# Kernel tuning notes

Hardware: AMD Instinct MI355X
Metric: run time of the kernel (lower is better)

The kernel has to match this reference:

```python
import jax, jax.numpy as jnp
import numpy as np

N, E, D, S, H, R = 16384, 262144, 64, 16, 8, 64
DH = D * H  # 512, tp2 output width (num_heads * node feature dim)
DOUT = 64
EPS = 1e-6


def _layernorm(x, g, b):
    mu = jnp.mean(x, axis=-1, keepdims=True)
    var = jnp.mean(jnp.square(x - mu), axis=-1, keepdims=True)
    return (x - mu) * jax.lax.rsqrt(var + EPS) * g + b


def setup_inputs() -> dict:
    key = jax.random.key(0)
    ks = jax.random.split(key, 16)
    rn = lambda k, shape, scale: jax.random.normal(k, shape, dtype=jnp.float32) * scale
    inp = {
        "node_fea": rn(ks[0], (N, D), 1.0),
        "edge_sh": rn(ks[1], (E, S), 1.0),
        "edge_length_embedding": rn(ks[2], (E, R), 1.0),
        "edge_src": jax.random.randint(ks[3], (E,), 0, N, dtype=jnp.int32),
        "edge_dst": jax.random.randint(ks[4], (E,), 0, N, dtype=jnp.int32),
        "batch": jnp.zeros((N,), dtype=jnp.int32),
        # pre_lin: Linear(D + D + R -> D)
        "W_pre": rn(ks[5], (D + D + R, D), 1.0 / np.sqrt(D + D + R)),
        "b_pre": jnp.zeros((D,), jnp.float32),
        # tp2 (EquiConv): tensor-product weights + radial gating MLP 64->64->DH
        "W_tp2": rn(ks[6], (D, S, DH), 1.0 / np.sqrt(D * S)),
        "r1": rn(ks[7], (R, R), 1.0 / np.sqrt(R)),
        "rb1": jnp.zeros((R,), jnp.float32),
        "r2": rn(ks[8], (R, DH), 1.0 / np.sqrt(R)),
        "rb2": jnp.zeros((DH,), jnp.float32),
        # lin_alpha: 64 -> 64 LN SiLU -> 64 LN SiLU -> H
        "a1": rn(ks[9], (R, R), 1.0 / np.sqrt(R)),
        "ab1": jnp.zeros((R,), jnp.float32),
        "g1": jnp.ones((R,), jnp.float32),
        "be1": jnp.zeros((R,), jnp.float32),
        "a2": rn(ks[10], (R, R), 1.0 / np.sqrt(R)),
        "ab2": jnp.zeros((R,), jnp.float32),
        "g2": jnp.ones((R,), jnp.float32),
        "be2": jnp.zeros((R,), jnp.float32),
        "a3": rn(ks[11], (R, H), 1.0 / np.sqrt(R)),
        "ab3": jnp.zeros((H,), jnp.float32),
        # lin: Linear(D*H -> DOUT)
        "W_lin": rn(ks[12], (DH, DOUT), 1.0 / np.sqrt(DH)),
        "b_lin": jnp.zeros((DOUT,), jnp.float32),
    }
    return inp


def reference(node_fea, edge_sh, edge_length_embedding, edge_src, edge_dst, batch,
              W_pre, b_pre, W_tp2, r1, rb1, r2, rb2,
              a1, ab1, g1, be1, a2, ab2, g2, be2, a3, ab3, W_lin, b_lin):
    n_nodes = node_fea.shape[0]
    # gather src/dst node features, concat radial embedding, pre_lin
    msg = jnp.concatenate(
        [node_fea[edge_src], node_fea[edge_dst], edge_length_embedding], axis=-1)
    msg = msg @ W_pre + b_pre  # [E, D]
    # EquiConv tp2: (msg tensor-product sh) contracted with learned weights,
    # gated per output channel by a radial MLP.
    gate = jax.nn.silu(edge_length_embedding @ r1 + rb1) @ r2 + rb2  # [E, DH]
    xs = jnp.einsum('ei,es->eis', msg, edge_sh).reshape(msg.shape[0], D * S)
    value = (xs @ W_tp2.reshape(D * S, DH)) * gate  # [E, DH]
    value = value.reshape(value.shape[0], H, D)  # [E, H, D]
    # attention logits from radial embedding
    h = jax.nn.silu(_layernorm(edge_length_embedding @ a1 + ab1, g1, be1))
    h = jax.nn.silu(_layernorm(h @ a2 + ab2, g2, be2))
    alpha = h @ a3 + ab3  # [E, H]
    # per-destination-node softmax over incoming edges
    m = jax.ops.segment_max(alpha, edge_dst, num_segments=n_nodes)
    ea = jnp.exp(alpha - m[edge_dst])
    denom = jax.ops.segment_sum(ea, edge_dst, num_segments=n_nodes)
    alpha = ea / denom[edge_dst]  # [E, H]
    # weight values and scatter-sum into destination nodes
    edge_fea = value * alpha[..., None]  # [E, H, D]
    node_agg = jax.ops.segment_sum(edge_fea, edge_dst, num_segments=n_nodes)
    out = node_agg.reshape(n_nodes, H * D) @ W_lin + b_lin  # [N, DOUT]
    return out
```

## Files before the change

### kernel.cpp

```cpp
#include <hip/hip_runtime.h>
#include <cstdint>
#include <cstddef>


typedef unsigned int u32;
typedef unsigned short u16;
typedef __attribute__((ext_vector_type(8))) short short8;
typedef __attribute__((ext_vector_type(4))) float f32x4;
typedef __attribute__((ext_vector_type(4))) u32 u32x4;

__device__ __forceinline__ float bf2f(u16 u){ return __uint_as_float(((u32)u)<<16); }
__device__ __forceinline__ u16 f2bf(float f){
  u32 i = __float_as_uint(f);
  u32 r = i + 0x7FFFu + ((i>>16)&1u);
  return (u16)(r>>16);
}
__device__ __forceinline__ u32 pk2(float a, float b){
  return (u32)f2bf(a) | ((u32)f2bf(b)<<16);
}
__device__ __forceinline__ u32 cvtpk(float a, float b){
  u32 r;
  asm("v_cvt_pk_bf16_f32 %0, %1, %2" : "=v"(r) : "v"(a), "v"(b));
  return r;
}
__device__ __forceinline__ void atomAddF(float* p, float v){
  asm volatile("global_atomic_add_f32 %0, %1, off" :: "v"(p), "v"(v) : "memory");
}
__device__ __forceinline__ void gl2lds(const void* g, void* l){
  __builtin_amdgcn_global_load_lds((const __attribute__((address_space(1))) u32*)g,
                                   (__attribute__((address_space(3))) u32*)l, 16, 0, 0);
}
__device__ __forceinline__ float decm(u32 k){
  u32 b = (k & 0x80000000u) ? (k & 0x7FFFFFFFu) : ~k;
  return __uint_as_float(b);
}

__global__ void k_prep(float* __restrict__ out, const float* __restrict__ bl,
                       u32* __restrict__ mkey, float* __restrict__ denom,
                       const float* __restrict__ W2, u16* __restrict__ w2t,
                       const float* __restrict__ r2, u16* __restrict__ r2t,
                       const float* __restrict__ Wl, u16* __restrict__ wlt)
{
  int t = blockIdx.x*256 + threadIdx.x;
  if (t < 1048576){ out[t] = bl[t&63]; return; }
  t -= 1048576;
  if (t < 131072){ mkey[t] = 0u; return; }
  t -= 131072;
  if (t < 131072){ denom[t] = 0.f; return; }
  t -= 131072;
  if (t < 65536){
    int o = t & 511, kc = t >> 9;
    u32x4 v;
    v.x = pk2(W2[(size_t)(kc*8+0)*512+o], W2[(size_t)(kc*8+1)*512+o]);
    v.y = pk2(W2[(size_t)(kc*8+2)*512+o], W2[(size_t)(kc*8+3)*512+o]);
    v.z = pk2(W2[(size_t)(kc*8+4)*512+o], W2[(size_t)(kc*8+5)*512+o]);
    v.w = pk2(W2[(size_t)(kc*8+6)*512+o], W2[(size_t)(kc*8+7)*512+o]);
    *(u32x4*)((char*)w2t + (size_t)o*2048 + kc*16) = v;
    return;
  }
  t -= 65536;
  if (t < 4096){
    int o = t & 511, kc = t >> 9;
    u32x4 v;
    v.x = pk2(r2[(size_t)(kc*8+0)*512+o], r2[(size_t)(kc*8+1)*512+o]);
    v.y = pk2(r2[(size_t)(kc*8+2)*512+o], r2[(size_t)(kc*8+3)*512+o]);
    v.z = pk2(r2[(size_t)(kc*8+4)*512+o], r2[(size_t)(kc*8+5)*512+o]);
    v.w = pk2(r2[(size_t)(kc*8+6)*512+o], r2[(size_t)(kc*8+7)*512+o]);
    *(u32x4*)((char*)r2t + (size_t)o*128 + kc*16) = v;
    return;
  }
  t -= 4096;
  {
    int j = t & 63, kc = t >> 6;
    u32x4 v;
    v.x = pk2(Wl[(size_t)(kc*8+0)*64+j], Wl[(size_t)(kc*8+1)*64+j]);
    v.y = pk2(Wl[(size_t)(kc*8+2)*64+j], Wl[(size_t)(kc*8+3)*64+j]);
    v.z = pk2(Wl[(size_t)(kc*8+4)*64+j], Wl[(size_t)(kc*8+5)*64+j]);
    v.w = pk2(Wl[(size_t)(kc*8+6)*64+j], Wl[(size_t)(kc*8+7)*64+j]);
    *(u32x4*)((char*)wlt + (size_t)j*1024 + kc*16) = v;
  }
}

#define GEMV4(ACC, X, WBASE)                                                       \
  { const float* w_ = (WBASE);                                                     \
    _Pragma("unroll") for (int j=0;j<64;j++) ACC[j] = fmaf((X).x, w_[j],     ACC[j]); \
    _Pragma("unroll") for (int j=0;j<64;j++) ACC[j] = fmaf((X).y, w_[64+j],  ACC[j]); \
    _Pragma("unroll") for (int j=0;j<64;j++) ACC[j] = fmaf((X).z, w_[128+j], ACC[j]); \
    _Pragma("unroll") for (int j=0;j<64;j++) ACC[j] = fmaf((X).w, w_[192+j], ACC[j]); }

__global__ __launch_bounds__(256) void k_msg(
    const float* __restrict__ nf, const float* __restrict__ eleg,
    const int* __restrict__ esrc, const int* __restrict__ edst,
    const float* __restrict__ Wp, const float* __restrict__ bp,
    const float* __restrict__ r1, const float* __restrict__ rb1,
    u16* __restrict__ msgb, u16* __restrict__ hgb)
{
  const int e = blockIdx.x*256 + threadIdx.x;
  const int src = esrc[e];
  const int dst = edst[e];
  const float4* sr4 = (const float4*)(nf + (size_t)src*64);
  const float4* dr4 = (const float4*)(nf + (size_t)dst*64);
  const float4* er4 = (const float4*)(eleg + (size_t)e*64);

  float acc[64];
  #pragma unroll
  for (int j=0;j<64;j++) acc[j] = bp[j];
  for (int ic=0; ic<16; ++ic){ float4 x = sr4[ic]; GEMV4(acc, x, Wp + ic*256); }
  for (int ic=0; ic<16; ++ic){ float4 x = dr4[ic]; GEMV4(acc, x, Wp + 4096 + ic*256); }
  for (int ic=0; ic<16; ++ic){ float4 x = er4[ic]; GEMV4(acc, x, Wp + 8192 + ic*256); }
  {
    u32x4* md = (u32x4*)(msgb + (size_t)e*64);
    #pragma unroll
    for (int c=0;c<8;c++){
      u32x4 v;
      v.x = cvtpk(acc[8*c+0],acc[8*c+1]); v.y = cvtpk(acc[8*c+2],acc[8*c+3]);
      v.z = cvtpk(acc[8*c+4],acc[8*c+5]); v.w = cvtpk(acc[8*c+6],acc[8*c+7]);
      md[c] = v;
    }
  }
  #pragma unroll
  for (int j=0;j<64;j++) acc[j] = rb1[j];
  for (int ic=0; ic<16; ++ic){ float4 x = er4[ic]; GEMV4(acc, x, r1 + ic*256); }
  #pragma unroll
  for (int j=0;j<64;j++) acc[j] = acc[j] / (1.f + __expf(-acc[j]));
  {
    u32x4* hd = (u32x4*)(hgb + (size_t)e*64);
    #pragma unroll
    for (int c=0;c<8;c++){
      u32x4 v;
      v.x = cvtpk(acc[8*c+0],acc[8*c+1]); v.y = cvtpk(acc[8*c+2],acc[8*c+3]);
      v.z = cvtpk(acc[8*c+4],acc[8*c+5]); v.w = cvtpk(acc[8*c+6],acc[8*c+7]);
      hd[c] = v;
    }
  }
}

__global__ __launch_bounds__(256) void k_attn(
    const float* __restrict__ eleg, const int* __restrict__ edst,
    const float* __restrict__ a1, const float* __restrict__ ab1,
    const float* __restrict__ g1, const float* __restrict__ be1,
    const float* __restrict__ a2, const float* __restrict__ ab2,
    const float* __restrict__ g2, const float* __restrict__ be2,
    const float* __restrict__ a3, const float* __restrict__ ab3,
    float* __restrict__ eab, u32* __restrict__ mkey)
{
  const int e = blockIdx.x*256 + threadIdx.x;
  const int dst = edst[e];
  const float4* er4 = (const float4*)(eleg + (size_t)e*64);

  float u[64];
  #pragma unroll
  for (int j=0;j<64;j++) u[j] = ab1[j];
  for (int ic=0; ic<16; ++ic){ float4 x = er4[ic]; GEMV4(u, x, a1 + ic*256); }
  {
    float s = 0.f;
    #pragma unroll
    for (int j=0;j<64;j++) s += u[j];
    float mu = s * 0.015625f;
    float s2 = 0.f;
    #pragma unroll
    for (int j=0;j<64;j++){ float d = u[j]-mu; s2 = fmaf(d,d,s2); }
    float rs = rsqrtf(s2*0.015625f + 1e-6f);
    #pragma unroll
    for (int j=0;j<64;j++){
      float y = (u[j]-mu)*rs*g1[j] + be1[j];
      u[j] = y / (1.f + __expf(-y));
    }
  }
  float v[64];
  #pragma unroll
  for (int j=0;j<64;j++) v[j] = ab2[j];
  #pragma unroll
  for (int i=0;i<64;i++){
    float x = u[i];
    const float* w = a2 + i*64;
    #pragma unroll
    for (int j=0;j<64;j++) v[j] = fmaf(x, w[j], v[j]);
  }
  {
    float s = 0.f;
    #pragma unroll
    for (int j=0;j<64;j++) s += v[j];
    float mu = s * 0.015625f;
    float s2 = 0.f;
    #pragma unroll
    for (int j=0;j<64;j++){ float d = v[j]-mu; s2 = fmaf(d,d,s2); }
    float rs = rsqrtf(s2*0.015625f + 1e-6f);
    #pragma unroll
    for (int j=0;j<64;j++){
      float y = (v[j]-mu)*rs*g2[j] + be2[j];
      v[j] = y / (1.f + __expf(-y));
    }
  }
  float l[8];
  #pragma unroll
  for (int h=0;h<8;h++) l[h] = ab3[h];
  #pragma unroll
  for (int i=0;i<64;i++){
    float x = v[i];
    #pragma unroll
    for (int h=0;h<8;h++) l[h] = fmaf(x, a3[i*8+h], l[h]);
  }
  float4* ld = (float4*)(eab + (size_t)e*8);
  ld[0] = make_float4(l[0],l[1],l[2],l[3]);
  ld[1] = make_float4(l[4],l[5],l[6],l[7]);
  #pragma unroll
  for (int h=0;h<8;h++){
    u32 b = __float_as_uint(l[h]);
    u32 k = (b & 0x80000000u) ? ~b : (b | 0x80000000u);
    atomicMax(&mkey[(size_t)dst*8 + h], k);
  }
}

__global__ void k_ea(const int* __restrict__ edst, float* __restrict__ eab,
                     const u32* __restrict__ mkey, float* __restrict__ denom)
{
  int e = blockIdx.x*256 + threadIdx.x;
  int dst = edst[e];
  float4 l0 = ((const float4*)(eab + (size_t)e*8))[0];
  float4 l1 = ((const float4*)(eab + (size_t)e*8))[1];
  uint4 k0 = ((const uint4*)(mkey + (size_t)dst*8))[0];
  uint4 k1 = ((const uint4*)(mkey + (size_t)dst*8))[1];
  float e0 = __expf(l0.x - decm(k0.x));
  float e1 = __expf(l0.y - decm(k0.y));
  float e2 = __expf(l0.z - decm(k0.z));
  float e3 = __expf(l0.w - decm(k0.w));
  float e4 = __expf(l1.x - decm(k1.x));
  float e5 = __expf(l1.y - decm(k1.y));
  float e6 = __expf(l1.z - decm(k1.z));
  float e7 = __expf(l1.w - decm(k1.w));
  ((float4*)(eab + (size_t)e*8))[0] = make_float4(e0,e1,e2,e3);
  ((float4*)(eab + (size_t)e*8))[1] = make_float4(e4,e5,e6,e7);
  float* dn = denom + (size_t)dst*8;
  atomAddF(dn+0,e0); atomAddF(dn+1,e1); atomAddF(dn+2,e2); atomAddF(dn+3,e3);
  atomAddF(dn+4,e4); atomAddF(dn+5,e5); atomAddF(dn+6,e6); atomAddF(dn+7,e7);
}

__global__ void k_norm(const int* __restrict__ edst, float* __restrict__ eab,
                       const float* __restrict__ denom)
{
  int e = blockIdx.x*256 + threadIdx.x;
  int dst = edst[e];
  float4 a0 = ((const float4*)(eab + (size_t)e*8))[0];
  float4 a1 = ((const float4*)(eab + (size_t)e*8))[1];
  float4 d0 = ((const float4*)(denom + (size_t)dst*8))[0];
  float4 d1 = ((const float4*)(denom + (size_t)dst*8))[1];
  ((float4*)(eab + (size_t)e*8))[0] = make_float4(a0.x/d0.x, a0.y/d0.y, a0.z/d0.z, a0.w/d0.w);
  ((float4*)(eab + (size_t)e*8))[1] = make_float4(a1.x/d1.x, a1.y/d1.y, a1.z/d1.z, a1.w/d1.w);
}

#define FORM_A(KSP, AN) {                                                        \
  float f0_ = bf2f((u16)((mrow[KSP]>>mshift)&0xFFFFu));                          \
  u32x4 w0_, w1_;                                                                \
  w0_.x=cvtpk(f0_*shr[0], f0_*shr[1]);  w0_.y=cvtpk(f0_*shr[2], f0_*shr[3]);     \
  w0_.z=cvtpk(f0_*shr[4], f0_*shr[5]);  w0_.w=cvtpk(f0_*shr[6], f0_*shr[7]);     \
  w1_.x=cvtpk(f0_*shr[8], f0_*shr[9]);  w1_.y=cvtpk(f0_*shr[10],f0_*shr[11]);    \
  w1_.z=cvtpk(f0_*shr[12],f0_*shr[13]); w1_.w=cvtpk(f0_*shr[14],f0_*shr[15]);    \
  char* b_ = (AN) + erow*128; int r7_ = erow&7;                                  \
  *(u32x4*)(b_ + (((t4*2+0)^r7_)*16)) = w0_;                                     \
  *(u32x4*)(b_ + (((t4*2+1)^r7_)*16)) = w1_; }

#define STAGE_B(KSP, BN) {                                                       \
  _Pragma("unroll")                                                              \
  for (int c_=0;c_<2;c_++){                                                      \
    int cid_=c_*512+tid, row_=cid_>>3, ch_=cid_&7;                               \
    gl2lds((const char*)w2t + (size_t)(j0+row_)*2048 + (KSP)*128 + ((ch_^(row_&7))*16), \
           (BN) + c_*8192 + wub);                                                \
  } }

__global__ __launch_bounds__(512,2) void k_fused(
    const u16* __restrict__ msgb, const float* __restrict__ shg,
    const u16* __restrict__ w2t, const u16* __restrict__ hgb,
    const u16* __restrict__ r2t, const float* __restrict__ rb2,
    const float* __restrict__ alpha, const u16* __restrict__ wlt,
    const int* __restrict__ edst, float* __restrict__ out)
{
  __shared__ char lds[65536];
  const int tid = threadIdx.x;
  const int e0 = blockIdx.x*128;
  const int wave = tid>>6, lane = tid&63;
  const int wm = wave>>2, wn = wave&3;
  const int wub = (tid&448)*16;
  char* A0 = lds;
  char* A1 = lds+16384;
  char* B0 = lds+32768;
  char* B1 = lds+49152;

  const int erow = tid>>2, t4 = tid&3;
  const int et = e0 + erow;
  u32 mrow[16];
  {
    const u32* mp32 = (const u32*)(msgb + (size_t)et*64);
    #pragma unroll
    for (int ks=0; ks<16; ++ks) mrow[ks] = mp32[ks*2 + (t4>>1)];
  }
  const int mshift = (t4&1)*16;
  float shr[16];
  {
    const float4* sp = (const float4*)(shg + (size_t)et*16);
    float4 s0=sp[0], s1=sp[1], s2=sp[2], s3=sp[3];
    shr[0]=s0.x; shr[1]=s0.y; shr[2]=s0.z; shr[3]=s0.w;
    shr[4]=s1.x; shr[5]=s1.y; shr[6]=s1.z; shr[7]=s1.w;
    shr[8]=s2.x; shr[9]=s2.y; shr[10]=s2.z; shr[11]=s2.w;
    shr[12]=s3.x; shr[13]=s3.y; shr[14]=s3.z; shr[15]=s3.w;
  }

  f32x4 acc_o[4];
  #pragma unroll
  for (int n=0;n<4;n++) acc_o[n] = (f32x4){0.f,0.f,0.f,0.f};

  #pragma unroll 1
  for (int jb=0; jb<4; ++jb){
    const int j0 = jb*128;
    __syncthreads();
    #pragma unroll
    for (int c=0;c<2;c++){
      int cid=c*512+tid, row=cid>>3, ch=cid&7;
      gl2lds((const char*)hgb + (size_t)(e0+row)*128 + ((ch^(row&7))*16),
             A0 + c*8192 + wub);
    }
    #pragma unroll
    for (int c=0;c<2;c++){
      int cid=c*512+tid, row=cid>>3, ch=cid&7;
      gl2lds((const char*)r2t + (size_t)(j0+row)*128 + ((ch^(row&7))*16),
             B0 + c*8192 + wub);
    }
    __syncthreads();

    f32x4 scale[4][2];
    {
      f32x4 accs[4][2];
      #pragma unroll
      for (int a=0;a<4;a++){ accs[a][0]=(f32x4){0.f,0.f,0.f,0.f}; accs[a][1]=(f32x4){0.f,0.f,0.f,0.f}; }
      #pragma unroll
      for (int kk=0;kk<2;kk++){
        short8 af[4], bfv[2];
        int kc = kk*4 + (lane>>4);
        #pragma unroll
        for (int mt=0;mt<4;mt++){
          int r = wm*64 + mt*16 + (lane&15);
          af[mt] = *(const short8*)(A0 + r*128 + ((kc ^ (r&7))*16));
        }
        #pragma unroll
        for (int nt=0;nt<2;nt++){
          int r = wn*32 + nt*16 + (lane&15);
          bfv[nt] = *(const short8*)(B0 + r*128 + ((kc ^ (r&7))*16));
        }
        #pragma unroll
        for (int mt=0;mt<4;mt++)
          #pragma unroll
          for (int nt=0;nt<2;nt++)
            accs[mt][nt] = __builtin_amdgcn_mfma_f32_16x16x32_bf16(af[mt], bfv[nt], accs[mt][nt], 0,0,0);
      }
      const int h = jb*2 + (wn>>1);
      float alv[4][4];
      #pragma unroll
      for (int mt=0;mt<4;mt++)
        #pragma unroll
        for (int q=0;q<4;q++){
          int row = wm*64 + mt*16 + (lane>>4)*4 + q;
          alv[mt][q] = alpha[(size_t)(e0+row)*8 + h];
        }
      float rbv[2];
      #pragma unroll
      for (int nt=0;nt<2;nt++) rbv[nt] = rb2[j0 + wn*32 + nt*16 + (lane&15)];
      #pragma unroll
      for (int mt=0;mt<4;mt++)
        #pragma unroll
        for (int nt=0;nt<2;nt++)
          #pragma unroll
          for (int q=0;q<4;q++)
            scale[mt][nt][q] = (accs[mt][nt][q] + rbv[nt]) * alv[mt][q];
    }
    __syncthreads();

    FORM_A(0, A0);
    STAGE_B(0, B0);
    __syncthreads();

    f32x4 accv[4][2];
    #pragma unroll
    for (int a=0;a<4;a++){ accv[a][0]=(f32x4){0.f,0.f,0.f,0.f}; accv[a][1]=(f32x4){0.f,0.f,0.f,0.f}; }

    #pragma unroll 2
    for (int ks=0; ks<16; ++ks){
      char* Ac = (ks&1) ? A1 : A0;
      char* Bc = (ks&1) ? B1 : B0;
      char* An = (ks&1) ? A0 : A1;
      char* Bn = (ks&1) ? B0 : B1;
      if (ks < 15){
        STAGE_B(ks+1, Bn);
        FORM_A(ks+1, An);
      }
      #pragma unroll
      for (int kk=0;kk<2;kk++){
        short8 af[4], bfv[2];
        int kc = kk*4 + (lane>>4);
        #pragma unroll
        for (int mt=0;mt<4;mt++){
          int r = wm*64 + mt*16 + (lane&15);
          af[mt] = *(const short8*)(Ac + r*128 + ((kc ^ (r&7))*16));
        }
        #pragma unroll
        for (int nt=0;nt<2;nt++){
          int r = wn*32 + nt*16 + (lane&15);
          bfv[nt] = *(const short8*)(Bc + r*128 + ((kc ^ (r&7))*16));
        }
        __builtin_amdgcn_s_setprio(1);
        #pragma unroll
        for (int mt=0;mt<4;mt++)
          #pragma unroll
          for (int nt=0;nt<2;nt++)
            accv[mt][nt] = __builtin_amdgcn_mfma_f32_16x16x32_bf16(af[mt], bfv[nt], accv[mt][nt], 0,0,0);
        __builtin_amdgcn_s_setprio(0);
      }
      __syncthreads();
    }

    #pragma unroll
    for (int mt=0;mt<4;mt++)
      #pragma unroll
      for (int nt=0;nt<2;nt++){
        int col = wn*32 + nt*16 + (lane&15);
        int c16 = col>>3, cby = (col&7)*2;
        #pragma unroll
        for (int q=0;q<4;q++){
          int row = wm*64 + mt*16 + (lane>>4)*4 + q;
          *(u16*)(lds + row*256 + ((c16 ^ ((row&7)<<1))*16) + cby) =
              f2bf(accv[mt][nt][q] * scale[mt][nt][q]);
        }
      }
    __syncthreads();

    #pragma unroll
    for (int kk=0;kk<4;kk++){
      short8 a2f;
      {
        int r = wave*16 + (lane&15);
        int kc = kk*4 + (lane>>4);
        a2f = *(const short8*)(lds + r*256 + ((kc ^ ((r&7)<<1))*16));
      }
      #pragma unroll
      for (int nt=0;nt<4;nt++){
        int j = nt*16 + (lane&15);
        int k = j0 + kk*32 + (lane>>4)*8;
        short8 b2f = *(const short8*)((const char*)wlt + (size_t)j*1024 + (size_t)k*2);
        acc_o[nt] = __builtin_amdgcn_mfma_f32_16x16x32_bf16(a2f, b2f, acc_o[nt], 0,0,0);
      }
    }
  }

  #pragma unroll
  for (int q=0;q<4;q++){
    int r = wave*16 + (lane>>4)*4 + q;
    int n = edst[e0 + r];
    float* basep = out + (size_t)n*64;
    #pragma unroll
    for (int nt=0;nt<4;nt++){
      int col = nt*16 + (lane&15);
      atomAddF(basep + col, acc_o[nt][q]);
    }
  }
}

extern "C" void kernel_launch(void* const* d_in, const int* in_sizes, int n_in,
                              void* d_out, int out_size, void* d_ws, size_t ws_size,
                              hipStream_t stream)
{
  const float* nf  = (const float*)d_in[0];
  const float* shg = (const float*)d_in[1];
  const float* ele = (const float*)d_in[2];
  const int* esrc  = (const int*)d_in[3];
  const int* edst  = (const int*)d_in[4];
  const float* Wp  = (const float*)d_in[6];
  const float* bp  = (const float*)d_in[7];
  const float* W2  = (const float*)d_in[8];
  const float* r1  = (const float*)d_in[9];
  const float* rb1 = (const float*)d_in[10];
  const float* r2  = (const float*)d_in[11];
  const float* rb2 = (const float*)d_in[12];
  const float* a1  = (const float*)d_in[13];
  const float* ab1 = (const float*)d_in[14];
  const float* g1  = (const float*)d_in[15];
  const float* be1 = (const float*)d_in[16];
  const float* a2  = (const float*)d_in[17];
  const float* ab2 = (const float*)d_in[18];
  const float* g2  = (const float*)d_in[19];
  const float* be2 = (const float*)d_in[20];
  const float* a3  = (const float*)d_in[21];
  const float* ab3 = (const float*)d_in[22];
  const float* Wl  = (const float*)d_in[23];
  const float* bl  = (const float*)d_in[24];
  float* out = (float*)d_out;
  char* ws = (char*)d_ws;

  u16* msgb    = (u16*)(ws + 0);
  u16* hgb     = (u16*)(ws + 33554432);
  float* eab   = (float*)(ws + 67108864);
  u32* mkey    = (u32*)(ws + 75497472);
  float* denom = (float*)(ws + 76021760);
  u16* w2t     = (u16*)(ws + 76546048);
  u16* r2t     = (u16*)(ws + 77594624);
  u16* wlt     = (u16*)(ws + 77660160);

  k_prep<<<5408,256,0,stream>>>(out, bl, mkey, denom, W2, w2t, r2, r2t, Wl, wlt);
  k_msg<<<1024,256,0,stream>>>(nf, ele, esrc, edst, Wp, bp, r1, rb1, msgb, hgb);
  k_attn<<<1024,256,0,stream>>>(ele, edst, a1, ab1, g1, be1, a2, ab2, g2, be2,
                                a3, ab3, eab, mkey);
  k_ea<<<1024,256,0,stream>>>(edst, eab, mkey, denom);
  k_norm<<<1024,256,0,stream>>>(edst, eab, denom);
  k_fused<<<2048,512,0,stream>>>(msgb, shg, w2t, hgb, r2t, rb2, eab, wlt, edst, out);
}
```

Measured before the change: 1.079 ms.

## Triple-buffer B tiles with explicit waitcnt pipeline and coalesce W_lin layout

Replaces the double-buffered main GEMM loop with a fully unrolled 16-step pipeline. B is staged two k-steps ahead across three LDS buffers, and each step is gated by explicit vmcnt/lgkmcnt waits and a raw barrier. This hides more global-to-LDS latency, but grows LDS from 64KB to 80KB, which may reduce occupancy at two blocks per CU. It also transposes the W_lin bf16 layout so the second GEMM's B loads read contiguous 16-byte chunks per lane. Separately, the attention MLP packs its first hidden layer to bf16 to cut register pressure, which slightly lowers precision.

```diff
diff --git a/kernel.cpp b/kernel.cpp
--- a/kernel.cpp
+++ b/kernel.cpp
@@ -77,7 +77,7 @@
     v.y = pk2(Wl[(size_t)(kc*8+2)*64+j], Wl[(size_t)(kc*8+3)*64+j]);
     v.z = pk2(Wl[(size_t)(kc*8+4)*64+j], Wl[(size_t)(kc*8+5)*64+j]);
     v.w = pk2(Wl[(size_t)(kc*8+6)*64+j], Wl[(size_t)(kc*8+7)*64+j]);
-    *(u32x4*)((char*)wlt + (size_t)j*1024 + kc*16) = v;
+    *(u32x4*)((char*)wlt + (size_t)kc*1024 + j*16) = v;
   }
 }
 
@@ -148,11 +148,12 @@
   const int dst = edst[e];
   const float4* er4 = (const float4*)(eleg + (size_t)e*64);
 
-  float u[64];
-  #pragma unroll
-  for (int j=0;j<64;j++) u[j] = ab1[j];
-  for (int ic=0; ic<16; ++ic){ float4 x = er4[ic]; GEMV4(u, x, a1 + ic*256); }
-  {
+  u32 u_pk[32];
+  {
+    float u[64];
+    #pragma unroll
+    for (int j=0;j<64;j++) u[j] = ab1[j];
+    for (int ic=0; ic<16; ++ic){ float4 x = er4[ic]; GEMV4(u, x, a1 + ic*256); }
     float s = 0.f;
     #pragma unroll
     for (int j=0;j<64;j++) s += u[j];
@@ -166,13 +167,15 @@
       float y = (u[j]-mu)*rs*g1[j] + be1[j];
       u[j] = y / (1.f + __expf(-y));
     }
+    #pragma unroll
+    for (int j=0;j<32;j++) u_pk[j] = cvtpk(u[2*j], u[2*j+1]);
   }
   float v[64];
   #pragma unroll
   for (int j=0;j<64;j++) v[j] = ab2[j];
   #pragma unroll
   for (int i=0;i<64;i++){
-    float x = u[i];
+    float x = bf2f((u16)((u_pk[i>>1] >> ((i&1)*16)) & 0xFFFFu));
     const float* w = a2 + i*64;
     #pragma unroll
     for (int j=0;j<64;j++) v[j] = fmaf(x, w[j], v[j]);
@@ -268,6 +271,40 @@
            (BN) + c_*8192 + wub);                                                \
   } }
 
+#define KSTEP(KS, DOSTAGE, DOFORM, VMN) {                                        \
+  asm volatile("s_waitcnt vmcnt(" #VMN ")" ::: "memory");                        \
+  asm volatile("s_waitcnt lgkmcnt(0)" ::: "memory");                             \
+  __builtin_amdgcn_s_barrier();                                                  \
+  __builtin_amdgcn_sched_barrier(0);                                             \
+  if (DOSTAGE){ STAGE_B((KS)+2, BB[((KS)+2)%3]); }                               \
+  if (DOFORM){ FORM_A((KS)+1, ((((KS)+1)&1) ? A1 : A0)); }                       \
+  {                                                                              \
+    char* Ac = (((KS)&1) ? A1 : A0);                                             \
+    char* Bc = BB[(KS)%3];                                                       \
+    _Pragma("unroll")                                                            \
+    for (int kk=0;kk<2;kk++){                                                    \
+      short8 af[4], bfv[2];                                                      \
+      int kc = kk*4 + (lane>>4);                                                 \
+      _Pragma("unroll")                                                          \
+      for (int mt=0;mt<4;mt++){                                                  \
+        int r = wm*64 + mt*16 + (lane&15);                                       \
+        af[mt] = *(const short8*)(Ac + r*128 + ((kc ^ (r&7))*16));               \
+      }                                                                          \
+      _Pragma("unroll")                                                          \
+      for (int nt=0;nt<2;nt++){                                                  \
+        int r = wn*32 + nt*16 + (lane&15);                                       \
+        bfv[nt] = *(const short8*)(Bc + r*128 + ((kc ^ (r&7))*16));              \
+      }                                                                          \
+      __builtin_amdgcn_s_setprio(1);                                             \
+      _Pragma("unroll")                                                          \
+      for (int mt=0;mt<4;mt++)                                                   \
+        _Pragma("unroll")                                                        \
+        for (int nt=0;nt<2;nt++)                                                 \
+          accv[mt][nt] = __builtin_amdgcn_mfma_f32_16x16x32_bf16(af[mt], bfv[nt], accv[mt][nt], 0,0,0); \
+      __builtin_amdgcn_s_setprio(0);                                             \
+    }                                                                            \
+  } }
+
 __global__ __launch_bounds__(512,2) void k_fused(
     const u16* __restrict__ msgb, const float* __restrict__ shg,
     const u16* __restrict__ w2t, const u16* __restrict__ hgb,
@@ -275,7 +312,7 @@
     const float* __restrict__ alpha, const u16* __restrict__ wlt,
     const int* __restrict__ edst, float* __restrict__ out)
 {
-  __shared__ char lds[65536];
+  __shared__ char lds[81920];
   const int tid = threadIdx.x;
   const int e0 = blockIdx.x*128;
   const int wave = tid>>6, lane = tid&63;
@@ -283,8 +320,8 @@
   const int wub = (tid&448)*16;
   char* A0 = lds;
   char* A1 = lds+16384;
-  char* B0 = lds+32768;
-  char* B1 = lds+49152;
+  char* BB[3] = { lds+32768, lds+49152, lds+65536 };
+  char* VS = lds+32768;
 
   const int erow = tid>>2, t4 = tid&3;
   const int et = e0 + erow;
@@ -323,7 +360,7 @@
     for (int c=0;c<2;c++){
       int cid=c*512+tid, row=cid>>3, ch=cid&7;
       gl2lds((const char*)r2t + (size_t)(j0+row)*128 + ((ch^(row&7))*16),
-             B0 + c*8192 + wub);
+             BB[0] + c*8192 + wub);
     }
     __syncthreads();
 
@@ -344,7 +381,7 @@
         #pragma unroll
         for (int nt=0;nt<2;nt++){
           int r = wn*32 + nt*16 + (lane&15);
-          bfv[nt] = *(const short8*)(B0 + r*128 + ((kc ^ (r&7))*16));
+          bfv[nt] = *(const short8*)(BB[0] + r*128 + ((kc ^ (r&7))*16));
         }
         #pragma unroll
         for (int mt=0;mt<4;mt++)
@@ -375,48 +412,19 @@
     __syncthreads();
 
     FORM_A(0, A0);
-    STAGE_B(0, B0);
+    STAGE_B(0, BB[0]);
+    STAGE_B(1, BB[1]);
+
+    f32x4 accv[4][2];
+    #pragma unroll
+    for (int a=0;a<4;a++){ accv[a][0]=(f32x4){0.f,0.f,0.f,0.f}; accv[a][1]=(f32x4){0.f,0.f,0.f,0.f}; }
+
+    KSTEP( 0,1,1,2) KSTEP( 1,1,1,2) KSTEP( 2,1,1,2) KSTEP( 3,1,1,2)
+    KSTEP( 4,1,1,2) KSTEP( 5,1,1,2) KSTEP( 6,1,1,2) KSTEP( 7,1,1,2)
+    KSTEP( 8,1,1,2) KSTEP( 9,1,1,2) KSTEP(10,1,1,2) KSTEP(11,1,1,2)
+    KSTEP(12,1,1,2) KSTEP(13,1,1,2) KSTEP(14,0,1,2) KSTEP(15,0,0,0)
+
     __syncthreads();
-
-    f32x4 accv[4][2];
-    #pragma unroll
-    for (int a=0;a<4;a++){ accv[a][0]=(f32x4){0.f,0.f,0.f,0.f}; accv[a][1]=(f32x4){0.f,0.f,0.f,0.f}; }
-
-    #pragma unroll 2
-    for (int ks=0; ks<16; ++ks){
-      char* Ac = (ks&1) ? A1 : A0;
-      char* Bc = (ks&1) ? B1 : B0;
-      char* An = (ks&1) ? A0 : A1;
-      char* Bn = (ks&1) ? B0 : B1;
-      if (ks < 15){
-        STAGE_B(ks+1, Bn);
-        FORM_A(ks+1, An);
-      }
-      #pragma unroll
-      for (int kk=0;kk<2;kk++){
-        short8 af[4], bfv[2];
-        int kc = kk*4 + (lane>>4);
-        #pragma unroll
-        for (int mt=0;mt<4;mt++){
-          int r = wm*64 + mt*16 + (lane&15);
-          af[mt] = *(const short8*)(Ac + r*128 + ((kc ^ (r&7))*16));
-        }
-        #pragma unroll
-        for (int nt=0;nt<2;nt++){
-          int r = wn*32 + nt*16 + (lane&15);
-          bfv[nt] = *(const short8*)(Bc + r*128 + ((kc ^ (r&7))*16));
-        }
-        __builtin_amdgcn_s_setprio(1);
-        #pragma unroll
-        for (int mt=0;mt<4;mt++)
-          #pragma unroll
-          for (int nt=0;nt<2;nt++)
-            accv[mt][nt] = __builtin_amdgcn_mfma_f32_16x16x32_bf16(af[mt], bfv[nt], accv[mt][nt], 0,0,0);
-        __builtin_amdgcn_s_setprio(0);
-      }
-      __syncthreads();
-    }
-
     #pragma unroll
     for (int mt=0;mt<4;mt++)
       #pragma unroll
@@ -426,7 +434,7 @@
         #pragma unroll
         for (int q=0;q<4;q++){
           int row = wm*64 + mt*16 + (lane>>4)*4 + q;
-          *(u16*)(lds + row*256 + ((c16 ^ ((row&7)<<1))*16) + cby) =
+          *(u16*)(VS + row*256 + ((c16 ^ ((row&7)<<1))*16) + cby) =
               f2bf(accv[mt][nt][q] * scale[mt][nt][q]);
         }
       }
@@ -438,13 +446,13 @@
       {
         int r = wave*16 + (lane&15);
         int kc = kk*4 + (lane>>4);
-        a2f = *(const short8*)(lds + r*256 + ((kc ^ ((r&7)<<1))*16));
+        a2f = *(const short8*)(VS + r*256 + ((kc ^ ((r&7)<<1))*16));
       }
+      int kcg = jb*16 + kk*4 + (lane>>4);
       #pragma unroll
       for (int nt=0;nt<4;nt++){
-        int j = nt*16 + (lane&15);
-        int k = j0 + kk*32 + (lane>>4)*8;
-        short8 b2f = *(const short8*)((const char*)wlt + (size_t)j*1024 + (size_t)k*2);
+        short8 b2f = *(const short8*)((const char*)wlt + (size_t)kcg*1024
+                                      + (nt*16 + (lane&15))*16);
         acc_o[nt] = __builtin_amdgcn_mfma_f32_16x16x32_bf16(a2f, b2f, acc_o[nt], 0,0,0);
       }
     }
```

New measurement: 1.864 ms. 72.9% more time.
